# Optimization experiments

Measured on AMD Instinct MI355X. Metric: run time of the kernel, lower is better.

## Reference

```python
import jax, jax.numpy as jnp
import numpy as np

FILTER_WIDTH = 6


def setup_inputs() -> dict:
    key = jax.random.key(0)
    ks = jax.random.split(key, 9)
    V, E, H, C = 50000, 128, 128, 2
    B, S = 64, 512
    inputs = jax.random.randint(ks[0], (B, S), 0, V)
    lengths = jax.random.randint(ks[1], (B,), 1, S)
    embed_table = (jax.random.normal(ks[2], (V, E), jnp.float32) * 0.1).at[0].set(0.0)  # padding_idx=0
    s = 1.0 / np.sqrt(H)
    w_ih = jax.random.uniform(ks[3], (4 * H, E), jnp.float32, -s, s)
    w_hh = jax.random.uniform(ks[4], (4 * H, H), jnp.float32, -s, s)
    b_ih = jax.random.uniform(ks[5], (4 * H,), jnp.float32, -s, s)
    b_hh = jax.random.uniform(ks[6], (4 * H,), jnp.float32, -s, s)
    sf = 1.0 / np.sqrt(H)
    fc_w = jax.random.uniform(ks[7], (C, H), jnp.float32, -sf, sf)
    fc_b = jax.random.uniform(ks[8], (C,), jnp.float32, -sf, sf)
    return dict(inputs=inputs, lengths=lengths, embed_table=embed_table,
                w_ih=w_ih, w_hh=w_hh, b_ih=b_ih, b_hh=b_hh, fc_w=fc_w, fc_b=fc_b)


def reference(inputs, lengths, embed_table, w_ih, w_hh, b_ih, b_hh, fc_w, fc_b):
    # Dropouts are identity in eval mode (p set to 0).
    B, S = inputs.shape
    E = embed_table.shape[1]
    H = w_hh.shape[1]
    FW = FILTER_WIDTH
    W = S - FW + 1

    emb = embed_table[inputs]                                   # [B, S, E]
    idx = jnp.arange(W)[:, None] + jnp.arange(FW)[None, :]       # [W, FW]
    xw = emb[:, idx, :]                                          # [B, W, FW, E] sliding windows
    x = xw.reshape(B * W, FW, E).transpose(1, 0, 2)              # [FW, B*W, E] time-major

    bias = b_ih + b_hh

    def step(carry, xt):
        h, c = carry
        g = xt @ w_ih.T + h @ w_hh.T + bias                      # [B*W, 4H], gate order i,f,g,o
        i, f, gg, o = jnp.split(g, 4, axis=-1)
        c = jax.nn.sigmoid(f) * c + jax.nn.sigmoid(i) * jnp.tanh(gg)
        h = jax.nn.sigmoid(o) * jnp.tanh(c)
        return (h, c), None

    h0 = jnp.zeros((B * W, H), emb.dtype)
    (h_last, _), _ = jax.lax.scan(step, (h0, h0), x)             # final hidden per window
    feat = jnp.max(h_last.reshape(B, W, H), axis=1)              # max-pool over windows
    return feat @ fc_w.T + fc_b                                  # [B, num_class]
```

## Files before the change

### kernel.cpp

```cpp
#include <hip/hip_runtime.h>
#include <math.h>
#include <float.h>

#define Bn   64
#define Sn   512
#define FWn  6
#define Wn   507
#define WT   16
#define NTILE 32

#define PROWS   21
#define PSTRIDE 516

typedef __attribute__((ext_vector_type(8))) _Float16 half8;
typedef __attribute__((ext_vector_type(4))) _Float16 half4;
typedef __attribute__((ext_vector_type(4))) float f32x4;

__device__ __forceinline__ float sigf(float x)  {
    return __builtin_amdgcn_rcpf(1.0f + __expf(-x));
}
__device__ __forceinline__ float tanh_(float x) {
    return 1.0f - 2.0f * __builtin_amdgcn_rcpf(__expf(2.0f * x) + 1.0f);
}

__global__ void __launch_bounds__(256)
pack_w_kernel(const float* __restrict__ w_ih, const float* __restrict__ w_hh,
              _Float16* __restrict__ wih_p, _Float16* __restrict__ whh_p)
{
    const int idx = blockIdx.x * 256 + threadIdx.x;
    const int j  = idx & 7;
    const int L  = (idx >> 3) & 63;
    const int ks = (idx >> 9) & 3;
    const int nt = idx >> 11;
    const int row = nt * 16 + (L & 15);
    const int col = ks * 32 + (L >> 4) * 8 + j;
    wih_p[idx] = (_Float16)w_ih[row * 128 + col];
    whh_p[idx] = (_Float16)w_hh[row * 128 + col];
}

__global__ void __launch_bounds__(512)
lstm_kernel(const int* __restrict__ inputs, const float* __restrict__ embed,
            const _Float16* __restrict__ wih_p, const _Float16* __restrict__ whh_p,
            const float* __restrict__ b_ih, const float* __restrict__ b_hh,
            float* __restrict__ partial)
{
    __shared__ __align__(16) _Float16 Pt[PROWS * PSTRIDE];
    __shared__ __align__(16) _Float16 hsA[2][2048];
    const int t    = threadIdx.x;
    const int L    = t & 63;
    const int ut   = t >> 6;
    const int b    = blockIdx.x >> 5;
    const int tile = blockIdx.x & 31;
    const int w0   = tile * WT;
    const int q  = L >> 4;
    const int ln = L & 15;
    const int j8 = L & 7;
    const int u  = ut * 16 + ln;

    {
        f32x4 accx[2][4];
#pragma unroll
        for (int g = 0; g < 4; ++g) {
            const float bg = b_ih[g * 128 + u] + b_hh[g * 128 + u];
            accx[0][g] = (f32x4){bg, bg, bg, bg};
            accx[1][g] = accx[0][g];
        }
        int tok[2];
#pragma unroll
        for (int mt = 0; mt < 2; ++mt) {
            int s = w0 + mt * 16 + ln; s = s < 511 ? s : 511;
            tok[mt] = inputs[b * Sn + s];
        }
#pragma unroll
        for (int ks = 0; ks < 4; ++ks) {
            half8 ax[2];
#pragma unroll
            for (int mt = 0; mt < 2; ++mt) {
                const float* er = embed + (size_t)tok[mt] * 128 + ks * 32 + q * 8;
                float4 e0 = *(const float4*)er;
                float4 e1 = *(const float4*)(er + 4);
                half8 a;
                a[0] = (_Float16)e0.x; a[1] = (_Float16)e0.y;
                a[2] = (_Float16)e0.z; a[3] = (_Float16)e0.w;
                a[4] = (_Float16)e1.x; a[5] = (_Float16)e1.y;
                a[6] = (_Float16)e1.z; a[7] = (_Float16)e1.w;
                ax[mt] = a;
            }
#pragma unroll
            for (int g = 0; g < 4; ++g) {
                half8 bw = *(const half8*)(wih_p + ((size_t)((g * 8 + ut) * 4 + ks) * 64 + L) * 8);
                accx[0][g] = __builtin_amdgcn_mfma_f32_16x16x32_f16(ax[0], bw, accx[0][g], 0, 0, 0);
                accx[1][g] = __builtin_amdgcn_mfma_f32_16x16x32_f16(ax[1], bw, accx[1][g], 0, 0, 0);
            }
        }
#pragma unroll
        for (int mt = 0; mt < 2; ++mt)
#pragma unroll
            for (int r = 0; r < 4; ++r) {
                const int sl = mt * 16 + q * 4 + r;
                if (sl < PROWS) {
                    half4 o;
                    o[0] = (_Float16)accx[mt][0][r];
                    o[1] = (_Float16)accx[mt][1][r];
                    o[2] = (_Float16)accx[mt][2][r];
                    o[3] = (_Float16)accx[mt][3][r];
                    *(half4*)&Pt[sl * PSTRIDE + u * 4] = o;
                }
            }
    }

    half8 whf[4][4];
#pragma unroll
    for (int g = 0; g < 4; ++g)
#pragma unroll
        for (int ks = 0; ks < 4; ++ks)
            whf[g][ks] = *(const half8*)(whh_p + ((size_t)((g * 8 + ut) * 4 + ks) * 64 + L) * 8);

    __syncthreads();

    const int ks_h = ut >> 1;
    const int qp   = (ut & 1) * 2 + (ln >> 3);

    float cst[4] = {0.f, 0.f, 0.f, 0.f};
    float hh[4];

    for (int st = 0; st < FWn; ++st) {
        if (st > 0) __syncthreads();
        f32x4 acc[4];
#pragma unroll
        for (int r = 0; r < 4; ++r) {
            half4 pv = *(const half4*)&Pt[(q * 4 + r + st) * PSTRIDE + u * 4];
            acc[0][r] = (float)pv[0]; acc[1][r] = (float)pv[1];
            acc[2][r] = (float)pv[2]; acc[3][r] = (float)pv[3];
        }
        if (st > 0) {
            const _Float16* hb = hsA[(st + 1) & 1];
#pragma unroll
            for (int ks = 0; ks < 4; ++ks) {
                half8 ah = *(const half8*)(hb + (ks * 64 + L) * 8);
#pragma unroll
                for (int g = 0; g < 4; ++g)
                    acc[g] = __builtin_amdgcn_mfma_f32_16x16x32_f16(ah, whf[g][ks], acc[g], 0, 0, 0);
            }
        }
        _Float16* buf = hsA[st & 1];
#pragma unroll
        for (int r = 0; r < 4; ++r) {
            float ii = sigf(acc[0][r]);
            float ff = sigf(acc[1][r]);
            float gg = tanh_(acc[2][r]);
            float oo = sigf(acc[3][r]);
            float cc = ff * cst[r] + ii * gg;
            cst[r] = cc;
            hh[r] = oo * tanh_(cc);
            if (st < FWn - 1)
                buf[ks_h * 512 + (qp * 16 + q * 4 + r) * 8 + j8] = (_Float16)hh[r];
        }
    }

    float mv = -FLT_MAX;
#pragma unroll
    for (int r = 0; r < 4; ++r) {
        const int w = w0 + q * 4 + r;
        if (w < Wn) mv = fmaxf(mv, hh[r]);
    }
    mv = fmaxf(mv, __shfl_xor(mv, 16));
    mv = fmaxf(mv, __shfl_xor(mv, 32));
    if (q == 0)
        partial[(size_t)(b * NTILE + tile) * 128 + u] = mv;
}

__global__ void __launch_bounds__(128)
final_kernel(const float* __restrict__ partial, const float* __restrict__ fc_w,
             const float* __restrict__ fc_b, float* __restrict__ out)
{
    const int b = blockIdx.x;
    const int u = threadIdx.x;
    float m = -FLT_MAX;
#pragma unroll
    for (int tl = 0; tl < NTILE; ++tl)
        m = fmaxf(m, partial[(size_t)(b * NTILE + tl) * 128 + u]);
    float v0 = m * fc_w[u];
    float v1 = m * fc_w[128 + u];
#pragma unroll
    for (int off = 1; off < 64; off <<= 1) {
        v0 += __shfl_xor(v0, off);
        v1 += __shfl_xor(v1, off);
    }
    __shared__ float red[2][2];
    if ((u & 63) == 0) { red[u >> 6][0] = v0; red[u >> 6][1] = v1; }
    __syncthreads();
    if (u == 0) {
        out[b * 2 + 0] = red[0][0] + red[1][0] + fc_b[0];
        out[b * 2 + 1] = red[0][1] + red[1][1] + fc_b[1];
    }
}

extern "C" void kernel_launch(void* const* d_in, const int* in_sizes, int n_in,
                              void* d_out, int out_size, void* d_ws, size_t ws_size,
                              hipStream_t stream)
{
    const int*   inputs = (const int*)d_in[0];
    const float* embed  = (const float*)d_in[2];
    const float* w_ih   = (const float*)d_in[3];
    const float* w_hh   = (const float*)d_in[4];
    const float* b_ih   = (const float*)d_in[5];
    const float* b_hh   = (const float*)d_in[6];
    const float* fc_w   = (const float*)d_in[7];
    const float* fc_b   = (const float*)d_in[8];
    float* out = (float*)d_out;

    float*    partial = (float*)d_ws;
    _Float16* wih_p   = (_Float16*)(partial + Bn * NTILE * 128);
    _Float16* whh_p   = wih_p + 65536;

    pack_w_kernel<<<dim3(256), 256, 0, stream>>>(w_ih, w_hh, wih_p, whh_p);
    lstm_kernel<<<dim3(Bn * NTILE), 512, 0, stream>>>(inputs, embed, wih_p, whh_p,
                                                      b_ih, b_hh, partial);
    final_kernel<<<dim3(Bn), 128, 0, stream>>>(partial, fc_w, fc_b, out);
}
```

Baseline: 148.5 us.

## Process 32 windows per block with two independent 16-row LSTM sub-tiles

Doubles the window tile per block from 16 to 32, halving the block count to 1024. Each block now computes the input projection for 37 token rows, which cuts the redundant halo rows (5 per tile) and amortizes the W_hh register load and bias setup over more work. The recurrence processes two independent 16-row sub-tiles per step, which gives extra ILP between MFMA chains and the activation math. In exchange it uses more shared memory and registers per block, so occupancy may drop.

```diff
diff --git a/kernel.cpp b/kernel.cpp
--- a/kernel.cpp
+++ b/kernel.cpp
@@ -6,10 +6,10 @@
 #define Sn   512
 #define FWn  6
 #define Wn   507
-#define WT   16
-#define NTILE 32
-
-#define PROWS   21
+#define WT   32
+#define NTILE 16
+
+#define PROWS   37
 #define PSTRIDE 516
 
 typedef __attribute__((ext_vector_type(8))) _Float16 half8;
@@ -45,12 +45,12 @@
             float* __restrict__ partial)
 {
     __shared__ __align__(16) _Float16 Pt[PROWS * PSTRIDE];
-    __shared__ __align__(16) _Float16 hsA[2][2048];
+    __shared__ __align__(16) _Float16 hsA[2][2][2048];
     const int t    = threadIdx.x;
     const int L    = t & 63;
     const int ut   = t >> 6;
-    const int b    = blockIdx.x >> 5;
-    const int tile = blockIdx.x & 31;
+    const int b    = blockIdx.x >> 4;
+    const int tile = blockIdx.x & 15;
     const int w0   = tile * WT;
     const int q  = L >> 4;
     const int ln = L & 15;
@@ -58,24 +58,25 @@
     const int u  = ut * 16 + ln;
 
     {
-        f32x4 accx[2][4];
+        f32x4 accx[3][4];
 #pragma unroll
         for (int g = 0; g < 4; ++g) {
             const float bg = b_ih[g * 128 + u] + b_hh[g * 128 + u];
             accx[0][g] = (f32x4){bg, bg, bg, bg};
             accx[1][g] = accx[0][g];
-        }
-        int tok[2];
-#pragma unroll
-        for (int mt = 0; mt < 2; ++mt) {
+            accx[2][g] = accx[0][g];
+        }
+        int tok[3];
+#pragma unroll
+        for (int mt = 0; mt < 3; ++mt) {
             int s = w0 + mt * 16 + ln; s = s < 511 ? s : 511;
             tok[mt] = inputs[b * Sn + s];
         }
 #pragma unroll
         for (int ks = 0; ks < 4; ++ks) {
-            half8 ax[2];
-#pragma unroll
-            for (int mt = 0; mt < 2; ++mt) {
+            half8 ax[3];
+#pragma unroll
+            for (int mt = 0; mt < 3; ++mt) {
                 const float* er = embed + (size_t)tok[mt] * 128 + ks * 32 + q * 8;
                 float4 e0 = *(const float4*)er;
                 float4 e1 = *(const float4*)(er + 4);
@@ -89,12 +90,13 @@
 #pragma unroll
             for (int g = 0; g < 4; ++g) {
                 half8 bw = *(const half8*)(wih_p + ((size_t)((g * 8 + ut) * 4 + ks) * 64 + L) * 8);
-                accx[0][g] = __builtin_amdgcn_mfma_f32_16x16x32_f16(ax[0], bw, accx[0][g], 0, 0, 0);
-                accx[1][g] = __builtin_amdgcn_mfma_f32_16x16x32_f16(ax[1], bw, accx[1][g], 0, 0, 0);
-            }
-        }
-#pragma unroll
-        for (int mt = 0; mt < 2; ++mt)
+#pragma unroll
+                for (int mt = 0; mt < 3; ++mt)
+                    accx[mt][g] = __builtin_amdgcn_mfma_f32_16x16x32_f16(ax[mt], bw, accx[mt][g], 0, 0, 0);
+            }
+        }
+#pragma unroll
+        for (int mt = 0; mt < 3; ++mt)
 #pragma unroll
             for (int r = 0; r < 4; ++r) {
                 const int sl = mt * 16 + q * 4 + r;
@@ -121,49 +123,54 @@
     const int ks_h = ut >> 1;
     const int qp   = (ut & 1) * 2 + (ln >> 3);
 
-    float cst[4] = {0.f, 0.f, 0.f, 0.f};
-    float hh[4];
+    float cst[2][4] = {{0.f, 0.f, 0.f, 0.f}, {0.f, 0.f, 0.f, 0.f}};
+    float hh[2][4];
 
     for (int st = 0; st < FWn; ++st) {
         if (st > 0) __syncthreads();
-        f32x4 acc[4];
+#pragma unroll
+        for (int sub = 0; sub < 2; ++sub) {
+            f32x4 acc[4];
+#pragma unroll
+            for (int r = 0; r < 4; ++r) {
+                half4 pv = *(const half4*)&Pt[(sub * 16 + q * 4 + r + st) * PSTRIDE + u * 4];
+                acc[0][r] = (float)pv[0]; acc[1][r] = (float)pv[1];
+                acc[2][r] = (float)pv[2]; acc[3][r] = (float)pv[3];
+            }
+            if (st > 0) {
+                const _Float16* hb = hsA[(st + 1) & 1][sub];
+#pragma unroll
+                for (int ks = 0; ks < 4; ++ks) {
+                    half8 ah = *(const half8*)(hb + (ks * 64 + L) * 8);
+#pragma unroll
+                    for (int g = 0; g < 4; ++g)
+                        acc[g] = __builtin_amdgcn_mfma_f32_16x16x32_f16(ah, whf[g][ks], acc[g], 0, 0, 0);
+                }
+            }
+            _Float16* buf = hsA[st & 1][sub];
+#pragma unroll
+            for (int r = 0; r < 4; ++r) {
+                float ii = sigf(acc[0][r]);
+                float ff = sigf(acc[1][r]);
+                float gg = tanh_(acc[2][r]);
+                float oo = sigf(acc[3][r]);
+                float cc = ff * cst[sub][r] + ii * gg;
+                cst[sub][r] = cc;
+                hh[sub][r] = oo * tanh_(cc);
+                if (st < FWn - 1)
+                    buf[ks_h * 512 + (qp * 16 + q * 4 + r) * 8 + j8] = (_Float16)hh[sub][r];
+            }
+        }
+    }
+
+    float mv = -FLT_MAX;
+#pragma unroll
+    for (int sub = 0; sub < 2; ++sub)
 #pragma unroll
         for (int r = 0; r < 4; ++r) {
-            half4 pv = *(const half4*)&Pt[(q * 4 + r + st) * PSTRIDE + u * 4];
-            acc[0][r] = (float)pv[0]; acc[1][r] = (float)pv[1];
-            acc[2][r] = (float)pv[2]; acc[3][r] = (float)pv[3];
-        }
-        if (st > 0) {
-            const _Float16* hb = hsA[(st + 1) & 1];
-#pragma unroll
-            for (int ks = 0; ks < 4; ++ks) {
-                half8 ah = *(const half8*)(hb + (ks * 64 + L) * 8);
-#pragma unroll
-                for (int g = 0; g < 4; ++g)
-                    acc[g] = __builtin_amdgcn_mfma_f32_16x16x32_f16(ah, whf[g][ks], acc[g], 0, 0, 0);
-            }
-        }
-        _Float16* buf = hsA[st & 1];
-#pragma unroll
-        for (int r = 0; r < 4; ++r) {
-            float ii = sigf(acc[0][r]);
-            float ff = sigf(acc[1][r]);
-            float gg = tanh_(acc[2][r]);
-            float oo = sigf(acc[3][r]);
-            float cc = ff * cst[r] + ii * gg;
-            cst[r] = cc;
-            hh[r] = oo * tanh_(cc);
-            if (st < FWn - 1)
-                buf[ks_h * 512 + (qp * 16 + q * 4 + r) * 8 + j8] = (_Float16)hh[r];
-        }
-    }
-
-    float mv = -FLT_MAX;
-#pragma unroll
-    for (int r = 0; r < 4; ++r) {
-        const int w = w0 + q * 4 + r;
-        if (w < Wn) mv = fmaxf(mv, hh[r]);
-    }
+            const int w = w0 + sub * 16 + q * 4 + r;
+            if (w < Wn) mv = fmaxf(mv, hh[sub][r]);
+        }
     mv = fmaxf(mv, __shfl_xor(mv, 16));
     mv = fmaxf(mv, __shfl_xor(mv, 32));
     if (q == 0)
```

Result: faster. 140.3 us, median of 2 (-5.5%).
